# Optimization experiments

Measured on AMD Instinct MI355X. Metric: run time of the kernel, lower is better.

Reference implementation:

```python
import jax, jax.numpy as jnp
import numpy as np

WS = (2, 7, 7)          # window size (s, h, w)
DIM = 192
HEADS = 6
HEAD_DIM = DIM // HEADS
N = WS[0] * WS[1] * WS[2]  # 98
TABLE = (2 * WS[0] - 1) * (2 * WS[1] - 1) * (2 * WS[2] - 1)  # 507


def _relative_position_index():
    coords = np.stack(np.meshgrid(np.arange(WS[0]), np.arange(WS[1]), np.arange(WS[2]), indexing='ij'))
    cf = coords.reshape(3, -1)                      # [3, N]
    rel = cf[:, :, None] - cf[:, None, :]           # [3, N, N]
    rel = rel.transpose(1, 2, 0).astype(np.int64)   # [N, N, 3]
    rel[..., 0] += WS[0] - 1
    rel[..., 1] += WS[1] - 1
    rel[..., 2] += WS[2] - 1
    rel[..., 0] *= 3 * WS[1] - 1  # faithful to source (quirky multiplier)
    rel[..., 1] *= 2 * WS[1] - 1
    return jnp.asarray(rel.sum(-1), dtype=jnp.int32)  # [N, N]


def setup_inputs() -> dict:
    key = jax.random.key(0)
    ks = jax.random.split(key, 8)
    B_ = 1024
    nW = 64
    skip = jax.random.normal(ks[0], (B_, N, DIM), dtype=jnp.float32)
    x_up = jax.random.normal(ks[1], (B_, N, DIM), dtype=jnp.float32)
    mask = jax.random.normal(ks[2], (nW, N, N), dtype=jnp.float32)
    kv_w = jax.random.normal(ks[3], (DIM, 2 * DIM), dtype=jnp.float32) * 0.02
    kv_b = jnp.zeros((2 * DIM,), dtype=jnp.float32)
    proj_w = jax.random.normal(ks[4], (DIM, DIM), dtype=jnp.float32) * 0.02
    proj_b = jnp.zeros((DIM,), dtype=jnp.float32)
    rpb_table = jax.random.normal(ks[5], (TABLE, HEADS), dtype=jnp.float32) * 0.02
    rel_idx = _relative_position_index()
    return {"skip": skip, "x_up": x_up, "mask": mask, "kv_w": kv_w, "kv_b": kv_b,
            "proj_w": proj_w, "proj_b": proj_b, "rpb_table": rpb_table, "rel_idx": rel_idx}


def reference(skip, x_up, mask, kv_w, kv_b, proj_w, proj_b, rpb_table, rel_idx):
    B_, n, C = skip.shape
    nW = mask.shape[0]
    scale = HEAD_DIM ** -0.5
    kv = skip @ kv_w + kv_b                                # [B_, N, 2C]
    kv = kv.reshape(B_, n, 2, HEADS, HEAD_DIM)
    k = kv[:, :, 0]                                        # [B_, N, H, hd]
    v = kv[:, :, 1]
    q = x_up.reshape(B_, n, HEADS, HEAD_DIM) * scale
    attn = jnp.einsum('bqhd,bkhd->bhqk', q, k)             # [B_, H, N, N]
    bias = rpb_table[rel_idx]                              # [N, N, H]
    attn = attn + jnp.transpose(bias, (2, 0, 1))[None]
    attn = attn.reshape(B_ // nW, nW, HEADS, n, n) + mask[None, :, None]
    attn = attn.reshape(B_, HEADS, n, n)
    attn = jax.nn.softmax(attn, axis=-1)
    out = jnp.einsum('bhqk,bkhd->bqhd', attn, v).reshape(B_, n, C)
    return out @ proj_w + proj_b
```

## Files before the change

kernel.cpp:

```cpp
#include <hip/hip_runtime.h>
#include <hip/hip_bf16.h>

#define NTOK 98
#define DIM 192
#define HEADS 6
#define SCALE 0.17677669529663687f

using shortx8 = __attribute__((ext_vector_type(8))) short;
using floatx4 = __attribute__((ext_vector_type(4))) float;

static __device__ __forceinline__ unsigned short f2bf(float f) {
    unsigned u = __float_as_uint(f);
    u += 0x7FFFu + ((u >> 16) & 1u);
    return (unsigned short)(u >> 16);
}

static __device__ __forceinline__ shortx8 pack8(const float* p, float scale) {
    float4 a = *(const float4*)p;
    float4 b = *(const float4*)(p + 4);
    shortx8 t;
    t[0] = (short)f2bf(a.x * scale); t[1] = (short)f2bf(a.y * scale);
    t[2] = (short)f2bf(a.z * scale); t[3] = (short)f2bf(a.w * scale);
    t[4] = (short)f2bf(b.x * scale); t[5] = (short)f2bf(b.y * scale);
    t[6] = (short)f2bf(b.z * scale); t[7] = (short)f2bf(b.w * scale);
    return t;
}

__global__ void prep_kernel(const float* __restrict__ rpb, const int* __restrict__ relidx,
                            const float* __restrict__ kvw, const float* __restrict__ pw,
                            float* __restrict__ biasF, unsigned short* __restrict__ kvB,
                            unsigned short* __restrict__ pB) {
    int e = blockIdx.x * 256 + threadIdx.x;
    if (e < HEADS * NTOK * NTOK) {
        int h = e / (NTOK * NTOK), ij = e % (NTOK * NTOK);
        biasF[e] = rpb[relidx[ij] * HEADS + h];
    }
    if (e < 73728) {
        int jj = e & 7, lane = (e >> 3) & 63, t = e >> 9;
        int NT = t % 24, ks = t / 24;
        int c = ks * 32 + (lane >> 4) * 8 + jj;
        int n = NT * 16 + (lane & 15);
        kvB[e] = f2bf(kvw[c * 384 + n]);
    }
    if (e < 36864) {
        int jj = e & 7, lane = (e >> 3) & 63, t = e >> 9;
        int NT = t % 12, ks = t / 12;
        int c = ks * 32 + (lane >> 4) * 8 + jj;
        int n = NT * 16 + (lane & 15);
        pB[e] = f2bf(pw[c * 192 + n]);
    }
}

__global__ __launch_bounds__(448, 4) void attn_kernel(
    const float* __restrict__ skip, const float* __restrict__ xup,
    const float* __restrict__ mask, const float* __restrict__ kv_b,
    const float* __restrict__ biasF, const unsigned short* __restrict__ kvB,
    float* __restrict__ o_out) {

    __shared__ unsigned short kB3[3 * 7 * 512];
    __shared__ unsigned short vB3[3 * 2 * 4 * 512];
    __shared__ unsigned short PA[7 * 4 * 512];

    const int tid  = threadIdx.x;
    const int w    = tid >> 6;
    const int lane = tid & 63;
    const int l15  = lane & 15;
    const int quad = lane >> 4;
    const int win  = blockIdx.x >> 1;
    const int g    = blockIdx.x & 1;

    for (int e = tid; e < 6 * 512; e += 448)
        vB3[(e / 512) * 4 * 512 + 3 * 512 + (e & 511)] = 0;
    for (int e = tid; e < 7 * 256; e += 448)
        PA[(e / 256) * 4 * 512 + 3 * 512 + 256 + (e & 255)] = 0;
    __syncthreads();

    const int mA  = w * 16 + l15;
    const int mAc = mA < NTOK ? mA : 97;

    shortx8 afr[6];
    {
        const float* sr = skip + ((size_t)win * NTOK + mAc) * DIM + quad * 8;
        #pragma unroll
        for (int ks = 0; ks < 6; ++ks) afr[ks] = pack8(sr + ks * 32, 1.0f);
    }
    #pragma unroll
    for (int nt = 0; nt < 12; ++nt) {
        const int NTg = (nt < 6) ? (6 * g + nt) : (6 + 6 * g + nt);
        const int col = NTg * 16 + l15;
        const float cb = kv_b[col];
        floatx4 acc = {cb, cb, cb, cb};
        #pragma unroll
        for (int ks = 0; ks < 6; ++ks) {
            shortx8 bf = *(const shortx8*)(kvB + ((size_t)((ks * 24 + NTg) * 64 + lane)) * 8);
            acc = __builtin_amdgcn_mfma_f32_16x16x32_bf16(afr[ks], bf, acc, 0, 0, 0);
        }
        if (nt < 6) {
            const int ch = nt * 16 + l15, hh = ch >> 5, dh = ch & 31;
            const int base = ((hh * 7 + w) * 64) * 8 + (dh & 7);
            const int lphi = ((dh >> 3) & 3) << 4;
            #pragma unroll
            for (int r = 0; r < 4; ++r) {
                int mm = quad * 4 + r;
                kB3[base + (mm | lphi) * 8] = f2bf(acc[r]);
            }
        } else {
            const int cv = (nt - 6) * 16 + l15, hh = cv >> 5, dh = cv & 31, ntv = dh >> 4;
            #pragma unroll
            for (int r = 0; r < 4; ++r) {
                int m = w * 16 + quad * 4 + r;
                if (m < NTOK) {
                    int lp = (dh & 15) | (((m >> 3) & 3) << 4);
                    vB3[(((hh * 2 + ntv) * 4 + (m >> 5)) * 64 + lp) * 8 + (m & 7)] = f2bf(acc[r]);
                }
            }
        }
    }
    __syncthreads();

    const float* mw = mask + (size_t)(win & 63) * NTOK * NTOK;

    for (int hp = 0; hp < 3; ++hp) {
        const int h = 3 * g + hp;
        shortx8 qf;
        {
            const float* xr = xup + ((size_t)win * NTOK + mAc) * DIM + h * 32 + quad * 8;
            qf = pack8(xr, SCALE);
        }
        floatx4 S[7];
        const float* bh = biasF + h * NTOK * NTOK;
        #pragma unroll
        for (int nt = 0; nt < 7; ++nt) {
            const int j = nt * 16 + l15;
            #pragma unroll
            for (int r = 0; r < 4; ++r) {
                int i = w * 16 + quad * 4 + r;
                int ic = i < NTOK ? i : 97;
                S[nt][r] = (j < NTOK) ? (bh[ic * NTOK + j] + mw[ic * NTOK + j]) : -1e30f;
            }
        }
        #pragma unroll
        for (int nt = 0; nt < 7; ++nt) {
            shortx8 bk = *(const shortx8*)&kB3[((hp * 7 + nt) * 64 + lane) * 8];
            S[nt] = __builtin_amdgcn_mfma_f32_16x16x32_bf16(qf, bk, S[nt], 0, 0, 0);
        }
        float inv[4];
        #pragma unroll
        for (int r = 0; r < 4; ++r) {
            float mx = S[0][r];
            #pragma unroll
            for (int nt = 1; nt < 7; ++nt) mx = fmaxf(mx, S[nt][r]);
            mx = fmaxf(mx, __shfl_xor(mx, 1));
            mx = fmaxf(mx, __shfl_xor(mx, 2));
            mx = fmaxf(mx, __shfl_xor(mx, 4));
            mx = fmaxf(mx, __shfl_xor(mx, 8));
            float sm = 0.f;
            #pragma unroll
            for (int nt = 0; nt < 7; ++nt) { float ev = __expf(S[nt][r] - mx); S[nt][r] = ev; sm += ev; }
            sm += __shfl_xor(sm, 1);
            sm += __shfl_xor(sm, 2);
            sm += __shfl_xor(sm, 4);
            sm += __shfl_xor(sm, 8);
            inv[r] = 1.0f / sm;
        }
        #pragma unroll
        for (int nt = 0; nt < 7; ++nt) {
            const int j = nt * 16 + l15;
            const int ks = nt >> 1;
            const int lphi = ((j >> 3) & 3) << 4;
            #pragma unroll
            for (int r = 0; r < 4; ++r) {
                int mm = quad * 4 + r;
                PA[((w * 4 + ks) * 64 + (mm | lphi)) * 8 + (j & 7)] = f2bf(S[nt][r] * inv[r]);
            }
        }
        __syncthreads();
        shortx8 pa[4];
        #pragma unroll
        for (int ks = 0; ks < 4; ++ks)
            pa[ks] = *(const shortx8*)&PA[((w * 4 + ks) * 64 + lane) * 8];
        #pragma unroll
        for (int nt = 0; nt < 2; ++nt) {
            floatx4 o = {0.f, 0.f, 0.f, 0.f};
            #pragma unroll
            for (int ks = 0; ks < 4; ++ks) {
                shortx8 vb = *(const shortx8*)&vB3[(((hp * 2 + nt) * 4 + ks) * 64 + lane) * 8];
                o = __builtin_amdgcn_mfma_f32_16x16x32_bf16(pa[ks], vb, o, 0, 0, 0);
            }
            #pragma unroll
            for (int r = 0; r < 4; ++r) {
                int m = w * 16 + quad * 4 + r;
                if (m < NTOK)
                    o_out[((size_t)win * NTOK + m) * DIM + h * 32 + nt * 16 + l15] = o[r];
            }
        }
        __syncthreads();
    }
}

__global__ __launch_bounds__(448, 4) void proj_kernel(
    float* __restrict__ io, const unsigned short* __restrict__ pB,
    const float* __restrict__ pb) {
    const int tid  = threadIdx.x;
    const int w    = tid >> 6;
    const int lane = tid & 63;
    const int l15  = lane & 15;
    const int quad = lane >> 4;
    const int win  = blockIdx.x;

    float* base = io + (size_t)win * NTOK * DIM;
    const int mA  = w * 16 + l15;
    const int mAc = mA < NTOK ? mA : 97;

    shortx8 afr[6];
    {
        const float* ar = base + mAc * DIM + quad * 8;
        #pragma unroll
        for (int ks = 0; ks < 6; ++ks) afr[ks] = pack8(ar + ks * 32, 1.0f);
    }
    #pragma unroll
    for (int nt = 0; nt < 12; ++nt) {
        const int n = nt * 16 + l15;
        const float bb = pb[n];
        floatx4 acc = {bb, bb, bb, bb};
        #pragma unroll
        for (int ks = 0; ks < 6; ++ks) {
            shortx8 bf = *(const shortx8*)(pB + ((size_t)((ks * 12 + nt) * 64 + lane)) * 8);
            acc = __builtin_amdgcn_mfma_f32_16x16x32_bf16(afr[ks], bf, acc, 0, 0, 0);
        }
        #pragma unroll
        for (int r = 0; r < 4; ++r) {
            int m = w * 16 + quad * 4 + r;
            if (m < NTOK) base[m * DIM + n] = acc[r];
        }
    }
}

extern "C" void kernel_launch(void* const* d_in, const int* in_sizes, int n_in,
                              void* d_out, int out_size, void* d_ws, size_t ws_size,
                              hipStream_t stream) {
    const float* skip   = (const float*)d_in[0];
    const float* x_up   = (const float*)d_in[1];
    const float* mask   = (const float*)d_in[2];
    const float* kv_w   = (const float*)d_in[3];
    const float* kv_b   = (const float*)d_in[4];
    const float* proj_w = (const float*)d_in[5];
    const float* proj_b = (const float*)d_in[6];
    const float* rpb    = (const float*)d_in[7];
    const int*   relidx = (const int*)d_in[8];
    float* out = (float*)d_out;

    float*          biasF = (float*)d_ws;
    unsigned short* kvB   = (unsigned short*)((char*)d_ws + 230496);
    unsigned short* pB    = (unsigned short*)((char*)d_ws + 377952);

    prep_kernel<<<288, 256, 0, stream>>>(rpb, relidx, kv_w, proj_w, biasF, kvB, pB);
    attn_kernel<<<2048, 448, 0, stream>>>(skip, x_up, mask, kv_b, biasF, kvB, out);
    proj_kernel<<<1024, 448, 0, stream>>>(out, pB, proj_b);
}
```

Before: 336.4 us.

## Fuse attention and output projection into one per-window kernel with 14 waves

Merges the attention and projection kernels into a single kernel that handles one window per 896-thread block. Two waves share each 16-row tile, splitting K/V generation and heads between them. The attention output goes to LDS as bf16 and is fed straight into the projection MFMAs, so the fp32 intermediate no longer makes a round trip through global memory. In exchange, K/V for each head pair is recomputed in three phases with extra barriers. The larger block and LDS footprint (PA, OA buffers) may also lower occupancy.

```diff
diff --git a/kernel.cpp b/kernel.cpp
--- a/kernel.cpp
+++ b/kernel.cpp
@@ -51,32 +51,41 @@
     }
 }
 
-__global__ __launch_bounds__(448, 4) void attn_kernel(
+__global__ __launch_bounds__(896, 4) void fused_kernel(
     const float* __restrict__ skip, const float* __restrict__ xup,
     const float* __restrict__ mask, const float* __restrict__ kv_b,
     const float* __restrict__ biasF, const unsigned short* __restrict__ kvB,
-    float* __restrict__ o_out) {
-
-    __shared__ unsigned short kB3[3 * 7 * 512];
-    __shared__ unsigned short vB3[3 * 2 * 4 * 512];
-    __shared__ unsigned short PA[7 * 4 * 512];
-
-    const int tid  = threadIdx.x;
-    const int w    = tid >> 6;
-    const int lane = tid & 63;
-    const int l15  = lane & 15;
-    const int quad = lane >> 4;
-    const int win  = blockIdx.x >> 1;
-    const int g    = blockIdx.x & 1;
-
-    for (int e = tid; e < 6 * 512; e += 448)
-        vB3[(e / 512) * 4 * 512 + 3 * 512 + (e & 511)] = 0;
-    for (int e = tid; e < 7 * 256; e += 448)
-        PA[(e / 256) * 4 * 512 + 3 * 512 + 256 + (e & 255)] = 0;
-    __syncthreads();
+    const unsigned short* __restrict__ pB, const float* __restrict__ pb,
+    float* __restrict__ out) {
+
+    __shared__ unsigned short kB[2 * 7 * 512];
+    __shared__ unsigned short vB[2 * 2 * 4 * 512];
+    __shared__ unsigned short PA[14 * 4 * 512];
+    __shared__ unsigned short OA[7 * 6 * 512];
+
+    const int tid    = threadIdx.x;
+    const int waveid = tid >> 6;
+    const int lane   = tid & 63;
+    const int l15    = lane & 15;
+    const int quad   = lane >> 4;
+    const int w      = waveid >> 1;
+    const int p      = waveid & 1;
+    const int win    = blockIdx.x;
+
+    {
+        unsigned long long* z = (unsigned long long*)&PA[waveid * 2048 + 3 * 512 + 256];
+        z[lane] = 0ull;
+    }
+    if (waveid == 13) {
+        #pragma unroll
+        for (int s = 0; s < 4; ++s) {
+            uint4* z = (uint4*)&vB[(s * 4 + 3) * 512];
+            z[lane] = make_uint4(0, 0, 0, 0);
+        }
+    }
 
     const int mA  = w * 16 + l15;
-    const int mAc = mA < NTOK ? mA : 97;
+    const int mAc = mA < NTOK ? mA : NTOK - 1;
 
     shortx8 afr[6];
     {
@@ -84,49 +93,49 @@
         #pragma unroll
         for (int ks = 0; ks < 6; ++ks) afr[ks] = pack8(sr + ks * 32, 1.0f);
     }
-    #pragma unroll
-    for (int nt = 0; nt < 12; ++nt) {
-        const int NTg = (nt < 6) ? (6 * g + nt) : (6 + 6 * g + nt);
-        const int col = NTg * 16 + l15;
-        const float cb = kv_b[col];
-        floatx4 acc = {cb, cb, cb, cb};
-        #pragma unroll
-        for (int ks = 0; ks < 6; ++ks) {
-            shortx8 bf = *(const shortx8*)(kvB + ((size_t)((ks * 24 + NTg) * 64 + lane)) * 8);
-            acc = __builtin_amdgcn_mfma_f32_16x16x32_bf16(afr[ks], bf, acc, 0, 0, 0);
-        }
-        if (nt < 6) {
-            const int ch = nt * 16 + l15, hh = ch >> 5, dh = ch & 31;
-            const int base = ((hh * 7 + w) * 64) * 8 + (dh & 7);
-            const int lphi = ((dh >> 3) & 3) << 4;
-            #pragma unroll
-            for (int r = 0; r < 4; ++r) {
-                int mm = quad * 4 + r;
-                kB3[base + (mm | lphi) * 8] = f2bf(acc[r]);
-            }
-        } else {
-            const int cv = (nt - 6) * 16 + l15, hh = cv >> 5, dh = cv & 31, ntv = dh >> 4;
-            #pragma unroll
-            for (int r = 0; r < 4; ++r) {
-                int m = w * 16 + quad * 4 + r;
-                if (m < NTOK) {
-                    int lp = (dh & 15) | (((m >> 3) & 3) << 4);
-                    vB3[(((hh * 2 + ntv) * 4 + (m >> 5)) * 64 + lp) * 8 + (m & 7)] = f2bf(acc[r]);
+
+    const float* mw   = mask + (size_t)(win & 63) * NTOK * NTOK;
+    float*       base = out + (size_t)win * NTOK * DIM;
+
+    for (int a = 0; a < 3; ++a) {
+        if (a) __syncthreads();
+
+        #pragma unroll
+        for (int t = 0; t < 4; ++t) {
+            const int NT  = (p ? 12 : 0) + 4 * a + t;
+            const int col = NT * 16 + l15;
+            const float cb = kv_b[col];
+            floatx4 acc = {cb, cb, cb, cb};
+            #pragma unroll
+            for (int ks = 0; ks < 6; ++ks) {
+                shortx8 bf = *(const shortx8*)(kvB + ((size_t)((ks * 24 + NT) * 64 + lane)) * 8);
+                acc = __builtin_amdgcn_mfma_f32_16x16x32_bf16(afr[ks], bf, acc, 0, 0, 0);
+            }
+            const int cl = t * 16 + l15;
+            const int hh = cl >> 5, dh = cl & 31;
+            if (!p) {
+                const int bpos = (hh * 7 + w) * 512 + (dh & 7);
+                const int lphi = ((dh >> 3) & 3) << 4;
+                #pragma unroll
+                for (int r = 0; r < 4; ++r)
+                    kB[bpos + ((quad * 4 + r) | lphi) * 8] = f2bf(acc[r]);
+            } else {
+                const int ntv = dh >> 4;
+                #pragma unroll
+                for (int r = 0; r < 4; ++r) {
+                    int j = w * 16 + quad * 4 + r;
+                    if (j < NTOK) {
+                        int lp = (dh & 15) | (((j >> 3) & 3) << 4);
+                        vB[((hh * 2 + ntv) * 4 + (j >> 5)) * 512 + lp * 8 + (j & 7)] = f2bf(acc[r]);
+                    }
                 }
             }
         }
-    }
-    __syncthreads();
-
-    const float* mw = mask + (size_t)(win & 63) * NTOK * NTOK;
-
-    for (int hp = 0; hp < 3; ++hp) {
-        const int h = 3 * g + hp;
-        shortx8 qf;
-        {
-            const float* xr = xup + ((size_t)win * NTOK + mAc) * DIM + h * 32 + quad * 8;
-            qf = pack8(xr, SCALE);
-        }
+        __syncthreads();
+
+        const int h = 2 * a + p;
+        shortx8 qf = pack8(xup + ((size_t)win * NTOK + mAc) * DIM + h * 32 + quad * 8, SCALE);
+
         floatx4 S[7];
         const float* bh = biasF + h * NTOK * NTOK;
         #pragma unroll
@@ -135,13 +144,13 @@
             #pragma unroll
             for (int r = 0; r < 4; ++r) {
                 int i = w * 16 + quad * 4 + r;
-                int ic = i < NTOK ? i : 97;
+                int ic = i < NTOK ? i : NTOK - 1;
                 S[nt][r] = (j < NTOK) ? (bh[ic * NTOK + j] + mw[ic * NTOK + j]) : -1e30f;
             }
         }
         #pragma unroll
         for (int nt = 0; nt < 7; ++nt) {
-            shortx8 bk = *(const shortx8*)&kB3[((hp * 7 + nt) * 64 + lane) * 8];
+            shortx8 bk = *(const shortx8*)&kB[(p * 7 + nt) * 512 + lane * 8];
             S[nt] = __builtin_amdgcn_mfma_f32_16x16x32_bf16(qf, bk, S[nt], 0, 0, 0);
         }
         float inv[4];
@@ -163,70 +172,53 @@
             sm += __shfl_xor(sm, 8);
             inv[r] = 1.0f / sm;
         }
+        unsigned short* PAw = PA + waveid * 2048;
         #pragma unroll
         for (int nt = 0; nt < 7; ++nt) {
             const int j = nt * 16 + l15;
             const int ks = nt >> 1;
             const int lphi = ((j >> 3) & 3) << 4;
             #pragma unroll
-            for (int r = 0; r < 4; ++r) {
-                int mm = quad * 4 + r;
-                PA[((w * 4 + ks) * 64 + (mm | lphi)) * 8 + (j & 7)] = f2bf(S[nt][r] * inv[r]);
-            }
-        }
-        __syncthreads();
+            for (int r = 0; r < 4; ++r)
+                PAw[ks * 512 + ((quad * 4 + r) | lphi) * 8 + (j & 7)] = f2bf(S[nt][r] * inv[r]);
+        }
         shortx8 pa[4];
         #pragma unroll
         for (int ks = 0; ks < 4; ++ks)
-            pa[ks] = *(const shortx8*)&PA[((w * 4 + ks) * 64 + lane) * 8];
+            pa[ks] = *(const shortx8*)&PAw[ks * 512 + lane * 8];
         #pragma unroll
         for (int nt = 0; nt < 2; ++nt) {
             floatx4 o = {0.f, 0.f, 0.f, 0.f};
             #pragma unroll
             for (int ks = 0; ks < 4; ++ks) {
-                shortx8 vb = *(const shortx8*)&vB3[(((hp * 2 + nt) * 4 + ks) * 64 + lane) * 8];
+                shortx8 vb = *(const shortx8*)&vB[((p * 2 + nt) * 4 + ks) * 512 + lane * 8];
                 o = __builtin_amdgcn_mfma_f32_16x16x32_bf16(pa[ks], vb, o, 0, 0, 0);
             }
+            const int kbase = h * 32 + nt * 16 + l15;
+            const int lphi  = ((kbase >> 3) & 3) << 4;
             #pragma unroll
             for (int r = 0; r < 4; ++r) {
-                int m = w * 16 + quad * 4 + r;
-                if (m < NTOK)
-                    o_out[((size_t)win * NTOK + m) * DIM + h * 32 + nt * 16 + l15] = o[r];
-            }
-        }
-        __syncthreads();
-    }
-}
-
-__global__ __launch_bounds__(448, 4) void proj_kernel(
-    float* __restrict__ io, const unsigned short* __restrict__ pB,
-    const float* __restrict__ pb) {
-    const int tid  = threadIdx.x;
-    const int w    = tid >> 6;
-    const int lane = tid & 63;
-    const int l15  = lane & 15;
-    const int quad = lane >> 4;
-    const int win  = blockIdx.x;
-
-    float* base = io + (size_t)win * NTOK * DIM;
-    const int mA  = w * 16 + l15;
-    const int mAc = mA < NTOK ? mA : 97;
-
-    shortx8 afr[6];
-    {
-        const float* ar = base + mAc * DIM + quad * 8;
-        #pragma unroll
-        for (int ks = 0; ks < 6; ++ks) afr[ks] = pack8(ar + ks * 32, 1.0f);
-    }
+                int m = quad * 4 + r;
+                OA[(w * 6 + h) * 512 + (m | lphi) * 8 + (kbase & 7)] = f2bf(o[r]);
+            }
+        }
+    }
+    __syncthreads();
+
+    shortx8 ao[6];
     #pragma unroll
-    for (int nt = 0; nt < 12; ++nt) {
-        const int n = nt * 16 + l15;
+    for (int ks = 0; ks < 6; ++ks)
+        ao[ks] = *(const shortx8*)&OA[(w * 6 + ks) * 512 + lane * 8];
+    #pragma unroll
+    for (int t = 0; t < 6; ++t) {
+        const int nt = p * 6 + t;
+        const int n  = nt * 16 + l15;
         const float bb = pb[n];
         floatx4 acc = {bb, bb, bb, bb};
         #pragma unroll
         for (int ks = 0; ks < 6; ++ks) {
             shortx8 bf = *(const shortx8*)(pB + ((size_t)((ks * 12 + nt) * 64 + lane)) * 8);
-            acc = __builtin_amdgcn_mfma_f32_16x16x32_bf16(afr[ks], bf, acc, 0, 0, 0);
+            acc = __builtin_amdgcn_mfma_f32_16x16x32_bf16(ao[ks], bf, acc, 0, 0, 0);
         }
         #pragma unroll
         for (int r = 0; r < 4; ++r) {
@@ -255,6 +247,5 @@
     unsigned short* pB    = (unsigned short*)((char*)d_ws + 377952);
 
     prep_kernel<<<288, 256, 0, stream>>>(rpb, relidx, kv_w, proj_w, biasF, kvB, pB);
-    attn_kernel<<<2048, 448, 0, stream>>>(skip, x_up, mask, kv_b, biasF, kvB, out);
-    proj_kernel<<<1024, 448, 0, stream>>>(out, pB, proj_b);
-}
+    fused_kernel<<<1024, 896, 0, stream>>>(skip, x_up, mask, kv_b, biasF, kvB, pB, proj_b, out);
+}
```

Measured after the change: 497.0 us. +47.8%, slower.
